# Kernel optimization log

Hardware: AMD Instinct MI355X
Metric: run time of the kernel (lower is better)

## Reference

```python
import jax, jax.numpy as jnp
import numpy as np

H = 64  # GRU hidden size


def _gru_scan(x_proj, m, U, b_rec):
    # x_proj: [S,B,3H] precomputed input projections (time-major); m: [S,B] bool mask
    B = x_proj.shape[1]
    h0 = jnp.zeros((B, H), x_proj.dtype)

    def step(h, inp):
        xp, mt = inp
        rec = h @ U + b_rec                       # [B,3H] (Keras reset_after=True)
        xz, xr, xh = jnp.split(xp, 3, axis=-1)
        rz, rr, rh = jnp.split(rec, 3, axis=-1)
        z = jax.nn.sigmoid(xz + rz)
        r = jax.nn.sigmoid(xr + rr)
        hh = jnp.tanh(xh + r * rh)
        hn = z * h + (1.0 - z) * hh
        hn = jnp.where(mt[:, None], hn, h)        # masked steps carry state through
        return hn, hn

    hT, hs = jax.lax.scan(step, h0, (x_proj, m))
    return hs, hT  # hs: [S,B,H], hT: [B,H]


def setup_inputs() -> dict:
    key = jax.random.key(0)
    ks = jax.random.split(key, 16)
    V, E = 50000, 25
    B, S, T = 512, 200, 10
    s = 0.05
    f32 = jnp.float32
    inp = {
        "input_batch": jax.random.randint(ks[0], (B, S, T), 0, V),
        "emb_table": jax.random.normal(ks[1], (V, E), f32) * s,
        "W_f": jax.random.normal(ks[2], (E, 3 * H), f32) * s,
        "U_f": jax.random.normal(ks[3], (H, 3 * H), f32) * s,
        "b_f": jnp.zeros((2, 3 * H), f32),
        "W_b": jax.random.normal(ks[4], (E, 3 * H), f32) * s,
        "U_b": jax.random.normal(ks[5], (H, 3 * H), f32) * s,
        "b_b": jnp.zeros((2, 3 * H), f32),
        "W_k": jax.random.normal(ks[6], (2 * H, H), f32) * s,
        "b_k": jnp.zeros((H,), f32),
        "W_q": jax.random.normal(ks[7], (H, H), f32) * s,
        "b_q": jnp.zeros((H,), f32),
        "W_e": jax.random.normal(ks[8], (H, 1), f32) * s,
        "b_e": jnp.zeros((1,), f32),
    }
    return inp


def reference(input_batch, emb_table, W_f, U_f, b_f, W_b, U_b, b_b, W_k, b_k, W_q, b_q, W_e, b_e):
    mask = input_batch != 0                                  # [B,S,T]
    emb = emb_table[input_batch]                             # [B,S,T,E]
    nm = mask.astype(emb.dtype)
    denom = nm.sum(axis=2)                                   # [B,S]
    denom = jnp.where(denom == 0, jnp.ones_like(denom), denom)
    x = (emb * nm[..., None]).sum(axis=2) / denom[..., None] # [B,S,E] masked mean over tags
    step_mask = mask[:, :, 0]                                # [B,S] GRU step mask

    xT = jnp.swapaxes(x, 0, 1)                               # [S,B,E]
    mT = jnp.swapaxes(step_mask, 0, 1)                       # [S,B]

    # forward GRU
    hs_f, hT_f = _gru_scan(xT @ W_f + b_f[0], mT, U_f, b_f[1])
    # backward GRU: reverse time, scan, reverse back
    hs_b, _ = _gru_scan((xT @ W_b + b_b[0])[::-1], mT[::-1], U_b, b_b[1])
    hs_b = hs_b[::-1]

    out = jnp.swapaxes(jnp.concatenate([hs_f, hs_b], axis=-1), 0, 1)  # [B,S,2H]

    # Bahdanau attention; query = forward final state
    keys = out @ W_k + b_k                                   # [B,S,H]
    queries = hT_f @ W_q + b_q                               # [B,H]
    e = jnp.tanh(keys + queries[:, None, :]) @ W_e + b_e     # [B,S,1]
    e = e + (1.0 - step_mask.astype(e.dtype))[..., None] * -1e9
    w = jax.nn.softmax(e, axis=1)                            # [B,S,1]
    context = (w * out).sum(axis=1)                          # [B,2H]
    return context
```

## Files before the change

### kernel.cpp

```cpp
#include <hip/hip_runtime.h>
#include <math.h>

#define BATCH 512
#define SEQ   200
#define TOK   10
#define EMB   25
#define XPAD  28
#define HID   64
#define G3    192

__device__ __forceinline__ float fast_sigmoid(float t) {
    float e = __expf(-t);
    return __builtin_amdgcn_rcpf(1.f + e);
}
__device__ __forceinline__ float fast_tanh(float t) {
    float e2 = __expf(2.f * t);
    return 1.f - 2.f * __builtin_amdgcn_rcpf(e2 + 1.f);
}

#define LDS_BARRIER() do {                                   \
    asm volatile("s_waitcnt lgkmcnt(0)" ::: "memory");       \
    __builtin_amdgcn_s_barrier();                            \
    asm volatile("" ::: "memory");                           \
} while (0)

__global__ __launch_bounds__(256) void emb_mean_kernel(
    const int* __restrict__ ids_g, const float* __restrict__ emb,
    float* __restrict__ x, float* __restrict__ mask)
{
    int grp  = blockIdx.x * 8 + (threadIdx.x >> 5);
    int lane = threadIdx.x & 31;
    if (grp >= BATCH * SEQ) return;
    const int* ids = ids_g + (size_t)grp * TOK;
    float acc = 0.f;
    int cnt = 0;
    #pragma unroll
    for (int t = 0; t < TOK; t++) {
        int id = ids[t];
        if (id != 0) {
            cnt++;
            if (lane < EMB) acc += emb[(size_t)id * EMB + lane];
        }
    }
    if (lane < EMB)
        x[(size_t)grp * EMB + lane] = cnt ? acc / (float)cnt : 0.f;
    if (lane == 0)
        mask[grp] = (ids[0] != 0) ? 1.f : 0.f;
}


#define U_LIST(M) \
  M(0)  M(1)  M(2)  M(3)  M(4)  M(5)  M(6)  M(7)  \
  M(8)  M(9)  M(10) M(11) M(12) M(13) M(14) M(15) \
  M(16) M(17) M(18) M(19) M(20) M(21) M(22) M(23) \
  M(24) M(25) M(26) M(27) M(28) M(29) M(30) M(31) \
  M(32) M(33) M(34) M(35) M(36) M(37) M(38) M(39) \
  M(40) M(41) M(42) M(43) M(44) M(45) M(46) M(47) \
  M(48) M(49) M(50) M(51) M(52) M(53) M(54) M(55) \
  M(56) M(57) M(58) M(59) M(60) M(61) M(62) M(63)

#define W_LIST(M) \
  M(0)  M(1)  M(2)  M(3)  M(4)  M(5)  M(6)  M(7)  \
  M(8)  M(9)  M(10) M(11) M(12) M(13) M(14) M(15) \
  M(16) M(17) M(18) M(19) M(20) M(21) M(22) M(23) M(24)

#define DECL_U(i) const float u##i = U[(i) * G3 + col];
#define DECL_W(i) const float w##i = W[(i) * G3 + col];

#define REC4(q, i0, i1, i2, i3) {                 \
    const float4 hv = hs4[q];                     \
    a0 = fmaf(hv.x, u##i0, a0);                   \
    a1 = fmaf(hv.y, u##i1, a1);                   \
    a2 = fmaf(hv.z, u##i2, a2);                   \
    a3 = fmaf(hv.w, u##i3, a3); }

#define X4(q, i0, i1, i2, i3) {                   \
    const float4 xv = xr4[q];                     \
    p0 = fmaf(xv.x, w##i0, p0);                   \
    p1 = fmaf(xv.y, w##i1, p1);                   \
    p2 = fmaf(xv.z, w##i2, p2);                   \
    p3 = fmaf(xv.w, w##i3, p3); }

#define XPROJ(P, XR) do {                                         \
    const float4* xr4 = (const float4*)(XR);                      \
    float p0 = bx, p1 = 0.f, p2 = 0.f, p3 = 0.f;                  \
    X4(0, 0, 1, 2, 3)   X4(1, 4, 5, 6, 7)   X4(2, 8, 9, 10, 11)  \
    X4(3, 12, 13, 14, 15) X4(4, 16, 17, 18, 19) X4(5, 20, 21, 22, 23) \
    p0 = fmaf((XR)[24], w24, p0);                                 \
    P = (p0 + p1) + (p2 + p3);                                    \
} while (0)

__global__ __launch_bounds__(192)
__attribute__((amdgpu_waves_per_eu(4, 4)))
void gru_kernel(
    const float* __restrict__ xg, const float* __restrict__ maskg,
    const float* __restrict__ W_f, const float* __restrict__ U_f, const float* __restrict__ b_f,
    const float* __restrict__ W_b, const float* __restrict__ U_b, const float* __restrict__ b_b,
    float* __restrict__ outg, float* __restrict__ hT)
{
    const int bidx = blockIdx.x;
    const int dir  = bidx >> 9;
    const int b    = bidx & 511;
    const int tid  = threadIdx.x;
    const int w    = tid >> 6;
    const int j    = tid & 63;

    const float* W    = dir ? W_b : W_f;
    const float* U    = dir ? U_b : U_f;
    const float* bias = dir ? b_b : b_f;

    const int col = w * HID + j;

    U_LIST(DECL_U)
    W_LIST(DECL_W)
    const float bx = bias[col];
    const float br = bias[G3 + col];

    __shared__ __align__(16) float xs[SEQ * XPAD];
    __shared__ float ms[SEQ];
    __shared__ __align__(16) float hs[HID];
    __shared__ float zs[HID];
    __shared__ float rs[HID];

    {
        for (int i = tid; i < SEQ * EMB; i += 192) {
            int s = i / EMB;
            int e = i - s * EMB;
            xs[s * XPAD + e] = xg[(size_t)b * (SEQ * EMB) + i];
        }
        for (int i = tid; i < SEQ; i += 192) ms[i] = maskg[(size_t)b * SEQ + i];
        if (tid < HID) hs[tid] = 0.f;
    }
    __syncthreads();

    const float4* hs4 = (const float4*)hs;
    float h = 0.f;
    float* obase = outg + (size_t)b * SEQ * (2 * HID) + dir * HID + j;

    float p;
    {
        const int s0 = dir ? (SEQ - 1) : 0;
        XPROJ(p, xs + s0 * XPAD);
    }

    for (int step = 0; step < SEQ; step++) {
        const int s = dir ? (SEQ - 1 - step) : step;

        float a0 = br, a1 = 0.f, a2 = 0.f, a3 = 0.f;
        REC4(0,  0,  1,  2,  3)   REC4(1,  4,  5,  6,  7)
        REC4(2,  8,  9, 10, 11)   REC4(3, 12, 13, 14, 15)
        REC4(4, 16, 17, 18, 19)   REC4(5, 20, 21, 22, 23)
        REC4(6, 24, 25, 26, 27)   REC4(7, 28, 29, 30, 31)
        REC4(8, 32, 33, 34, 35)   REC4(9, 36, 37, 38, 39)
        REC4(10, 40, 41, 42, 43)  REC4(11, 44, 45, 46, 47)
        REC4(12, 48, 49, 50, 51)  REC4(13, 52, 53, 54, 55)
        REC4(14, 56, 57, 58, 59)  REC4(15, 60, 61, 62, 63)
        const float a = (a0 + a1) + (a2 + a3);

        if (w == 0)      zs[j] = fast_sigmoid(p + a);
        else if (w == 1) rs[j] = fast_sigmoid(p + a);

        LDS_BARRIER();

        if (w == 2) {
            float r  = rs[j];
            float z  = zs[j];
            float hh = fast_tanh(p + r * a);
            float hn = z * h + (1.f - z) * hh;
            hn = (ms[s] != 0.f) ? hn : h;
            h = hn;
            hs[j] = hn;
            obase[(size_t)s * (2 * HID)] = hn;
        }

        {
            const int sn  = dir ? (SEQ - 2 - step) : (step + 1);
            const int snc = (step + 1 < SEQ) ? sn : s;
            XPROJ(p, xs + snc * XPAD);
        }

        LDS_BARRIER();
    }
    if (w == 2 && dir == 0) hT[(size_t)b * HID + j] = h;
}

__global__ __launch_bounds__(256) void attn_kernel(
    const float* __restrict__ outg, const float* __restrict__ maskg,
    const float* __restrict__ hT,
    const float* __restrict__ W_k, const float* __restrict__ b_k,
    const float* __restrict__ W_q, const float* __restrict__ b_q,
    const float* __restrict__ W_e, const float* __restrict__ b_e,
    float* __restrict__ ctx)
{
    const int b   = blockIdx.x;
    const int tid = threadIdx.x;

    __shared__ float Wks[2 * HID * HID];
    __shared__ float qs[HID];
    __shared__ float es[SEQ];

    for (int i = tid; i < 2 * HID * HID; i += 256) Wks[i] = W_k[i];
    if (tid < HID) {
        float q = b_q[tid];
        const float* hrow = hT + (size_t)b * HID;
        #pragma unroll 8
        for (int i = 0; i < HID; i++) q = fmaf(hrow[i], W_q[i * HID + tid], q);
        qs[tid] = q;
    }
    __syncthreads();

    const int wave = tid >> 6;
    const int lane = tid & 63;
    const float bk = b_k[lane];
    const float we = W_e[lane];
    const float be = b_e[0];

    for (int s = wave; s < SEQ; s += 4) {
        const float* orow = outg + ((size_t)b * SEQ + s) * (2 * HID);
        float a0 = 0.f, a1 = 0.f, a2 = 0.f, a3 = 0.f;
        #pragma unroll
        for (int i = 0; i < 2 * HID; i += 4) {
            a0 = fmaf(orow[i + 0], Wks[(i + 0) * HID + lane], a0);
            a1 = fmaf(orow[i + 1], Wks[(i + 1) * HID + lane], a1);
            a2 = fmaf(orow[i + 2], Wks[(i + 2) * HID + lane], a2);
            a3 = fmaf(orow[i + 3], Wks[(i + 3) * HID + lane], a3);
        }
        float t = tanhf(((a0 + a1) + (a2 + a3)) + bk + qs[lane]) * we;
        #pragma unroll
        for (int off = 32; off > 0; off >>= 1) t += __shfl_down(t, off);
        if (lane == 0) {
            float pen = (maskg[(size_t)b * SEQ + s] != 0.f) ? 0.f : -1e9f;
            es[s] = t + be + pen;
        }
    }
    __syncthreads();

    if (tid < 64) {
        float mx = -1e30f;
        for (int s2 = tid; s2 < SEQ; s2 += 64) mx = fmaxf(mx, es[s2]);
        #pragma unroll
        for (int off = 32; off > 0; off >>= 1) mx = fmaxf(mx, __shfl_xor(mx, off));
        float sum = 0.f;
        for (int s2 = tid; s2 < SEQ; s2 += 64) {
            float w = expf(es[s2] - mx);
            es[s2] = w;
            sum += w;
        }
        #pragma unroll
        for (int off = 32; off > 0; off >>= 1) sum += __shfl_xor(sum, off);
        float inv = 1.f / sum;
        for (int s2 = tid; s2 < SEQ; s2 += 64) es[s2] *= inv;
    }
    __syncthreads();

    if (tid < 2 * HID) {
        const int jj = tid;
        float a0 = 0.f, a1 = 0.f;
        for (int s2 = 0; s2 < SEQ; s2 += 2) {
            a0 = fmaf(es[s2],     outg[((size_t)b * SEQ + s2)     * (2 * HID) + jj], a0);
            a1 = fmaf(es[s2 + 1], outg[((size_t)b * SEQ + s2 + 1) * (2 * HID) + jj], a1);
        }
        ctx[(size_t)b * (2 * HID) + jj] = a0 + a1;
    }
}

extern "C" void kernel_launch(void* const* d_in, const int* in_sizes, int n_in,
                              void* d_out, int out_size, void* d_ws, size_t ws_size,
                              hipStream_t stream) {
    const int*   ids = (const int*)  d_in[0];
    const float* emb = (const float*)d_in[1];
    const float* W_f = (const float*)d_in[2];
    const float* U_f = (const float*)d_in[3];
    const float* b_f = (const float*)d_in[4];
    const float* W_b = (const float*)d_in[5];
    const float* U_b = (const float*)d_in[6];
    const float* b_b = (const float*)d_in[7];
    const float* W_k = (const float*)d_in[8];
    const float* b_k = (const float*)d_in[9];
    const float* W_q = (const float*)d_in[10];
    const float* b_q = (const float*)d_in[11];
    const float* W_e = (const float*)d_in[12];
    const float* b_e = (const float*)d_in[13];

    float* ws   = (float*)d_ws;
    float* x    = ws;
    float* mask = ws + 2560000;
    float* out  = ws + 2662400;
    float* hT   = ws + 15769600;

    emb_mean_kernel<<<(BATCH * SEQ) / 8, 256, 0, stream>>>(ids, emb, x, mask);
    gru_kernel<<<1024, 192, 0, stream>>>(x, mask, W_f, U_f, b_f,
                                         W_b, U_b, b_b, out, hT);
    attn_kernel<<<BATCH, 256, 0, stream>>>(out, mask, hT, W_k, b_k,
                                           W_q, b_q, W_e, b_e, (float*)d_out);
}
```

Before: 432.1 us.

## Split GRU recurrent reduction across two waves per gate with LDS channel combine

Doubles the GRU block to 384 threads so that each gate column's recurrent dot product (K=64) and input projection (E=25) are split in half across two wavefronts. The partial sums go through an LDS channel array, and a single wave combines them with the folded biases to compute z, r and the new hidden state. This shortens the serial FMA chain per step and keeps fewer weights in registers per thread, which allows a higher waves-per-EU target. The cost is more LDS traffic per step, a wider barrier, and more serial work in the final combining wave.

After: 491.8 us. 13.8% more time.

```diff
diff --git a/kernel.cpp b/kernel.cpp
--- a/kernel.cpp
+++ b/kernel.cpp
@@ -49,49 +49,44 @@
 }
 
 
-#define U_LIST(M) \
+#define U32_LIST(M) \
   M(0)  M(1)  M(2)  M(3)  M(4)  M(5)  M(6)  M(7)  \
   M(8)  M(9)  M(10) M(11) M(12) M(13) M(14) M(15) \
   M(16) M(17) M(18) M(19) M(20) M(21) M(22) M(23) \
-  M(24) M(25) M(26) M(27) M(28) M(29) M(30) M(31) \
-  M(32) M(33) M(34) M(35) M(36) M(37) M(38) M(39) \
-  M(40) M(41) M(42) M(43) M(44) M(45) M(46) M(47) \
-  M(48) M(49) M(50) M(51) M(52) M(53) M(54) M(55) \
-  M(56) M(57) M(58) M(59) M(60) M(61) M(62) M(63)
-
-#define W_LIST(M) \
-  M(0)  M(1)  M(2)  M(3)  M(4)  M(5)  M(6)  M(7)  \
-  M(8)  M(9)  M(10) M(11) M(12) M(13) M(14) M(15) \
-  M(16) M(17) M(18) M(19) M(20) M(21) M(22) M(23) M(24)
-
-#define DECL_U(i) const float u##i = U[(i) * G3 + col];
-#define DECL_W(i) const float w##i = W[(i) * G3 + col];
-
-#define REC4(q, i0, i1, i2, i3) {                 \
+  M(24) M(25) M(26) M(27) M(28) M(29) M(30) M(31)
+
+#define W13_LIST(M) \
+  M(0) M(1) M(2) M(3) M(4) M(5) M(6) M(7) M(8) M(9) M(10) M(11) M(12)
+
+#define DECL_U(t) float u##t = U[(size_t)(kstart + (t)) * G3 + col];
+#define DECL_W(t) float w##t = ((t) < ne) ? W[(size_t)(estart + (t)) * G3 + col] : 0.f;
+#define PIN_U(t)  asm volatile("" : "+v"(u##t));
+#define PIN_W(t)  asm volatile("" : "+v"(w##t));
+
+#define RECQ(q, i0, i1, i2, i3) {                 \
     const float4 hv = hs4[q];                     \
     a0 = fmaf(hv.x, u##i0, a0);                   \
     a1 = fmaf(hv.y, u##i1, a1);                   \
-    a2 = fmaf(hv.z, u##i2, a2);                   \
-    a3 = fmaf(hv.w, u##i3, a3); }
-
-#define X4(q, i0, i1, i2, i3) {                   \
+    a0 = fmaf(hv.z, u##i2, a0);                   \
+    a1 = fmaf(hv.w, u##i3, a1); }
+
+#define XQ(q, i0, i1, i2, i3) {                   \
     const float4 xv = xr4[q];                     \
     p0 = fmaf(xv.x, w##i0, p0);                   \
     p1 = fmaf(xv.y, w##i1, p1);                   \
-    p2 = fmaf(xv.z, w##i2, p2);                   \
-    p3 = fmaf(xv.w, w##i3, p3); }
-
-#define XPROJ(P, XR) do {                                         \
-    const float4* xr4 = (const float4*)(XR);                      \
-    float p0 = bx, p1 = 0.f, p2 = 0.f, p3 = 0.f;                  \
-    X4(0, 0, 1, 2, 3)   X4(1, 4, 5, 6, 7)   X4(2, 8, 9, 10, 11)  \
-    X4(3, 12, 13, 14, 15) X4(4, 16, 17, 18, 19) X4(5, 20, 21, 22, 23) \
-    p0 = fmaf((XR)[24], w24, p0);                                 \
-    P = (p0 + p1) + (p2 + p3);                                    \
+    p0 = fmaf(xv.z, w##i2, p0);                   \
+    p1 = fmaf(xv.w, w##i3, p1); }
+
+#define XPROJ(P, XR) do {                                  \
+    const float4* xr4 = (const float4*)((XR) + estart);    \
+    float p0 = 0.f, p1 = 0.f;                              \
+    XQ(0, 0, 1, 2, 3)  XQ(1, 4, 5, 6, 7)  XQ(2, 8, 9, 10, 11) \
+    p0 = fmaf((XR)[estart + 12], w12, p0);                 \
+    P = p0 + p1;                                           \
 } while (0)
 
-__global__ __launch_bounds__(192)
-__attribute__((amdgpu_waves_per_eu(4, 4)))
+__global__ __launch_bounds__(384)
+__attribute__((amdgpu_waves_per_eu(6, 6)))
 void gru_kernel(
     const float* __restrict__ xg, const float* __restrict__ maskg,
     const float* __restrict__ W_f, const float* __restrict__ U_f, const float* __restrict__ b_f,
@@ -104,68 +99,77 @@
     const int tid  = threadIdx.x;
     const int w    = tid >> 6;
     const int j    = tid & 63;
+    const int g    = w >> 1;
+    const int kh   = w & 1;
 
     const float* W    = dir ? W_b : W_f;
     const float* U    = dir ? U_b : U_f;
     const float* bias = dir ? b_b : b_f;
 
-    const int col = w * HID + j;
-
-    U_LIST(DECL_U)
-    W_LIST(DECL_W)
-    const float bx = bias[col];
-    const float br = bias[G3 + col];
+    const int col    = g * HID + j;
+    const int kstart = kh * 32;
+    const int estart = kh * 12;
+    const int ne     = 12 + kh;
 
     __shared__ __align__(16) float xs[SEQ * XPAD];
     __shared__ float ms[SEQ];
     __shared__ __align__(16) float hs[HID];
-    __shared__ float zs[HID];
-    __shared__ float rs[HID];
-
-    {
-        for (int i = tid; i < SEQ * EMB; i += 192) {
-            int s = i / EMB;
-            int e = i - s * EMB;
-            xs[s * XPAD + e] = xg[(size_t)b * (SEQ * EMB) + i];
-        }
-        for (int i = tid; i < SEQ; i += 192) ms[i] = maskg[(size_t)b * SEQ + i];
-        if (tid < HID) hs[tid] = 0.f;
-    }
+    __shared__ float chan[8][HID];
+    __shared__ float bZs[HID], bRs[HID], bHXs[HID], bHRs[HID];
+
+    for (int i = tid; i < SEQ * EMB; i += 384) {
+        int s_ = i / EMB;
+        int e_ = i - s_ * EMB;
+        xs[s_ * XPAD + e_] = xg[(size_t)b * (SEQ * EMB) + i];
+    }
+    for (int i = tid; i < SEQ; i += 384) ms[i] = maskg[(size_t)b * SEQ + i];
+    if (tid < HID) {
+        hs[tid]   = 0.f;
+        bZs[tid]  = bias[tid] + bias[G3 + tid];
+        bRs[tid]  = bias[HID + tid] + bias[G3 + HID + tid];
+        bHXs[tid] = bias[2 * HID + tid];
+        bHRs[tid] = bias[G3 + 2 * HID + tid];
+    }
+
+    U32_LIST(DECL_U)
+    W13_LIST(DECL_W)
+    U32_LIST(PIN_U)
+    W13_LIST(PIN_W)
+
     __syncthreads();
 
-    const float4* hs4 = (const float4*)hs;
+    const float4* hs4 = (const float4*)(hs + kstart);
+    const int sdelta = dir ? -1 : 1;
+    int s = dir ? (SEQ - 1) : 0;
     float h = 0.f;
     float* obase = outg + (size_t)b * SEQ * (2 * HID) + dir * HID + j;
 
-    float p;
-    {
-        const int s0 = dir ? (SEQ - 1) : 0;
-        XPROJ(p, xs + s0 * XPAD);
-    }
+    float px;
+    XPROJ(px, xs + s * XPAD);
 
     for (int step = 0; step < SEQ; step++) {
-        const int s = dir ? (SEQ - 1 - step) : step;
-
-        float a0 = br, a1 = 0.f, a2 = 0.f, a3 = 0.f;
-        REC4(0,  0,  1,  2,  3)   REC4(1,  4,  5,  6,  7)
-        REC4(2,  8,  9, 10, 11)   REC4(3, 12, 13, 14, 15)
-        REC4(4, 16, 17, 18, 19)   REC4(5, 20, 21, 22, 23)
-        REC4(6, 24, 25, 26, 27)   REC4(7, 28, 29, 30, 31)
-        REC4(8, 32, 33, 34, 35)   REC4(9, 36, 37, 38, 39)
-        REC4(10, 40, 41, 42, 43)  REC4(11, 44, 45, 46, 47)
-        REC4(12, 48, 49, 50, 51)  REC4(13, 52, 53, 54, 55)
-        REC4(14, 56, 57, 58, 59)  REC4(15, 60, 61, 62, 63)
-        const float a = (a0 + a1) + (a2 + a3);
-
-        if (w == 0)      zs[j] = fast_sigmoid(p + a);
-        else if (w == 1) rs[j] = fast_sigmoid(p + a);
+        float a0 = 0.f, a1 = 0.f;
+        RECQ(0,  0,  1,  2,  3)   RECQ(1,  4,  5,  6,  7)
+        RECQ(2,  8,  9, 10, 11)   RECQ(3, 12, 13, 14, 15)
+        RECQ(4, 16, 17, 18, 19)   RECQ(5, 20, 21, 22, 23)
+        RECQ(6, 24, 25, 26, 27)   RECQ(7, 28, 29, 30, 31)
+        const float a = a0 + a1;
+
+        if (g < 2) {
+            chan[g * 2 + kh][j] = a + px;
+        } else {
+            chan[4 + kh][j] = px;
+            chan[6 + kh][j] = a;
+        }
 
         LDS_BARRIER();
 
-        if (w == 2) {
-            float r  = rs[j];
-            float z  = zs[j];
-            float hh = fast_tanh(p + r * a);
+        if (w == 4) {
+            float z  = fast_sigmoid(chan[0][j] + chan[1][j] + bZs[j]);
+            float r  = fast_sigmoid(chan[2][j] + chan[3][j] + bRs[j]);
+            float XH = chan[4][j] + chan[5][j] + bHXs[j];
+            float RH = chan[6][j] + chan[7][j] + bHRs[j];
+            float hh = fast_tanh(XH + r * RH);
             float hn = z * h + (1.f - z) * hh;
             hn = (ms[s] != 0.f) ? hn : h;
             h = hn;
@@ -174,14 +178,14 @@
         }
 
         {
-            const int sn  = dir ? (SEQ - 2 - step) : (step + 1);
-            const int snc = (step + 1 < SEQ) ? sn : s;
-            XPROJ(p, xs + snc * XPAD);
+            const int sn = (step < SEQ - 1) ? s + sdelta : s;
+            XPROJ(px, xs + sn * XPAD);
+            s = sn;
         }
 
         LDS_BARRIER();
     }
-    if (w == 2 && dir == 0) hT[(size_t)b * HID + j] = h;
+    if (w == 4 && dir == 0) hT[(size_t)b * HID + j] = h;
 }
 
 __global__ __launch_bounds__(256) void attn_kernel(
@@ -289,7 +293,7 @@
     float* hT   = ws + 15769600;
 
     emb_mean_kernel<<<(BATCH * SEQ) / 8, 256, 0, stream>>>(ids, emb, x, mask);
-    gru_kernel<<<1024, 192, 0, stream>>>(x, mask, W_f, U_f, b_f,
+    gru_kernel<<<1024, 384, 0, stream>>>(x, mask, W_f, U_f, b_f,
                                          W_b, U_b, b_b, out, hT);
     attn_kernel<<<BATCH, 256, 0, stream>>>(out, mask, hT, W_k, b_k,
                                            W_q, b_q, W_e, b_e, (float*)d_out);
```
